# Performance work log

Measured on AMD Instinct MI355X. Metric: run time of the kernel, lower is better.

Reference implementation:

```python
import jax, jax.numpy as jnp
import numpy as np
from jax import lax

I_CH = 3
C_CH = 2 * I_CH            # 6
PAIRS = [(i, j) for i in range(C_CH) for j in range(i + 1, C_CH)]  # 15 Givens pairs


def _encoder(x, W, b_enc):
    # CMEncoder stand-in: single SAME 3x3 conv in_channels -> out_channels
    y = lax.conv_general_dilated(x, W, (1, 1), 'SAME',
                                 dimension_numbers=('NCHW', 'OIHW', 'NCHW'))
    return y + b_enc[None, :, None, None]


def _covariance_matrix(s, a):
    # s: [b,C,h,w] per-pixel variances; a: [b,15,h,w] Givens angles
    d = jnp.moveaxis(s, 1, -1)      # [b,h,w,C]
    ang = jnp.moveaxis(a, 1, -1)    # [b,h,w,15]
    b, h, w, Cc = d.shape
    R = jnp.broadcast_to(jnp.eye(Cc, dtype=d.dtype), (b, h, w, Cc, Cc))
    for k, (i, j) in enumerate(PAIRS):
        c = jnp.cos(ang[..., k])[..., None]
        sn = jnp.sin(ang[..., k])[..., None]
        ci = R[..., :, i]
        cj = R[..., :, j]
        R = R.at[..., :, i].set(c * ci + sn * cj)
        R = R.at[..., :, j].set(-sn * ci + c * cj)
    # S = R diag(d) R^T  -> [b,h,w,C,C]
    S = jnp.einsum('bhwmk,bhwk,bhwnk->bhwmn', R, d, R)
    return S, R, d


def reference(x, W, b_enc):
    I = I_CH
    C = C_CH
    p = _encoder(x, W, b_enc)              # [b,30,h,w]
    m = p[:, :C]                           # means [b,6,h,w]
    s = p[:, C:2 * C]
    s = jnp.square(jax.nn.relu(s) - jax.nn.relu(-s))
    s = jnp.clip(s, 1e-6)
    a = 2.0 * jnp.pi * jax.nn.sigmoid(p[:, 2 * C:-I])
    xf = p[:, -I:]                         # [b,3,h,w]
    S, R, d = _covariance_matrix(s, a)
    # S^{-1} = R diag(1/d) R^T (D diagonal, R orthogonal) -> [b,h,w,6,6]
    S_1 = jnp.einsum('bhwmk,bhwk,bhwnk->bhwmn', R, 1.0 / d, R)
    Sxx = S_1[..., :I, :I]
    Syx = S_1[..., I:, :I]
    Q = jnp.matmul(Syx, jnp.linalg.inv(Sxx))   # [b,h,w,3,3]
    mx = m[:, :I]
    my = m[:, I:]
    y = my + jnp.einsum('bijmn,bnij->bmij', Q, xf - mx)
    Sout = jnp.transpose(S, (0, 3, 4, 1, 2))   # [b,6,6,h,w]
    return (xf, m, Sout, y)


def setup_inputs() -> dict:
    key = jax.random.key(0)
    k1, k2, k3 = jax.random.split(key, 3)
    x = jax.random.normal(k1, (4, 3, 256, 256), dtype=jnp.float32)
    W = jax.random.normal(k2, (30, 3, 3, 3), dtype=jnp.float32) * 0.1
    b_enc = jax.random.normal(k3, (30,), dtype=jnp.float32) * 0.1
    return {'x': x, 'W': W, 'b_enc': b_enc}
```

## Files before the change

### kernel.cpp

```cpp
#include <hip/hip_runtime.h>
#include <math.h>

#define HWp 65536

typedef float v2f __attribute__((ext_vector_type(2)));

__device__ __forceinline__ v2f fma2(v2f a, v2f b, v2f c) {
    return __builtin_elementwise_fma(a, b, c);
}

__global__ __launch_bounds__(128, 6)
void gp_encoder_kernel(const float* __restrict__ x,
                       const float* __restrict__ Wt,
                       const float* __restrict__ be,
                       float* __restrict__ out)
{
    __shared__ float Dsh[6][64];
    __shared__ float Ssh[18][64];

    const int lane = threadIdx.x & 63;
    const int wid  = threadIdx.x >> 6;

    const int blk  = blockIdx.x;
    const int b    = blk >> 10;
    const int pixb = (blk & 1023) << 6;
    const int h    = pixb >> 8;
    const int w0   = pixb & 255;

    const bool wlo_ok = !(w0 == 0   && lane == 0);
    const bool whi_ok = !(w0 == 192 && lane == 63);
    const int  idx_m1 = wlo_ok ? lane - 1 : lane;
    const int  idx_p1 = whi_ok ? lane + 1 : lane;

    float xs[27];
    const float* xb = x + b * 3 * HWp;
    #pragma unroll
    for (int ci = 0; ci < 3; ++ci) {
        #pragma unroll
        for (int kh = 0; kh < 3; ++kh) {
            const int hh = h + kh - 1;
            float v0 = 0.f, v1 = 0.f, v2 = 0.f;
            if ((unsigned)hh < 256u) {
                const float* rp = xb + ci * HWp + hh * 256 + w0;
                v0 = rp[idx_m1];
                v1 = rp[lane];
                v2 = rp[idx_p1];
                v0 = wlo_ok ? v0 : 0.f;
                v2 = whi_ok ? v2 : 0.f;
            }
            xs[ci*9 + kh*3 + 0] = v0;
            xs[ci*9 + kh*3 + 1] = v1;
            xs[ci*9 + kh*3 + 2] = v2;
        }
    }
    v2f xp[13];
    #pragma unroll
    for (int q = 0; q < 13; ++q)
        xp[q] = (v2f){xs[2*q], xs[2*q + 1]};
    const float x26 = xs[26];

    float* out_xf = out                      + b*3*HWp  + pixb;
    float* out_m  = out + 4*3*HWp            + b*6*HWp  + pixb;
    float* out_S  = out + (4*3+4*6)*HWp      + b*36*HWp + pixb;
    float* out_y  = out + (4*3+4*6+4*36)*HWp + b*3*HWp  + pixb;

    float pb[15];

    if (wid == 0) {
        float pa[15];
        #pragma unroll
        for (int o = 0; o < 15; ++o) {
            const int base = (12 + o) * 27;
            v2f acc2 = (v2f){0.f, 0.f};
            #pragma unroll
            for (int q = 0; q < 13; ++q) {
                v2f wq;
                wq.x = Wt[base + 2*q];
                wq.y = Wt[base + 2*q + 1];
                acc2 = fma2(xp[q], wq, acc2);
            }
            const float r = be[12 + o] + acc2.x + acc2.y;
            pa[o] = fmaf(x26, Wt[base + 26], r);
        }

        v2f Rc[6][3];
        #pragma unroll
        for (int c = 0; c < 6; ++c)
            #pragma unroll
            for (int p = 0; p < 3; ++p)
                Rc[c][p] = (v2f){(2*p == c) ? 1.f : 0.f, (2*p + 1 == c) ? 1.f : 0.f};

        const int PI_[15] = {0,0,0,0,0,1,1,1,1,2,2,2,3,3,4};
        const int PJ_[15] = {1,2,3,4,5,2,3,4,5,3,4,5,4,5,5};
        #pragma unroll
        for (int k = 0; k < 15; ++k) {
            const int i = PI_[k], j = PJ_[k];
            const float e  = __expf(-pa[k]);
            const float sg = __builtin_amdgcn_rcpf(1.f + e);
            const float c  = __builtin_amdgcn_cosf(sg);
            const float sn = __builtin_amdgcn_sinf(sg);
            const v2f c2 = (v2f){c, c};
            const v2f s2 = (v2f){sn, sn};
            #pragma unroll
            for (int p = 0; p < 3; ++p) {
                const v2f ri = Rc[i][p], rj = Rc[j][p];
                Rc[i][p] = fma2(c2, ri, s2 * rj);
                Rc[j][p] = fma2(c2, rj, -(s2 * ri));
            }
        }

        __syncthreads();

        float dk[6];
        #pragma unroll
        for (int k = 0; k < 6; ++k)
            dk[k] = Dsh[k][lane];

        #pragma unroll
        for (int n = 0; n < 6; ++n) {
            float t[6];
            #pragma unroll
            for (int k = 0; k < 6; ++k) {
                const float rnk = (n & 1) ? Rc[k][n >> 1].y : Rc[k][n >> 1].x;
                t[k] = dk[k] * rnk;
            }
            v2f col[3];
            #pragma unroll
            for (int p = 0; p < 3; ++p) {
                v2f acc = Rc[0][p] * (v2f){t[0], t[0]};
                #pragma unroll
                for (int k = 1; k < 6; ++k)
                    acc = fma2(Rc[k][p], (v2f){t[k], t[k]}, acc);
                col[p] = acc;
            }
            #pragma unroll
            for (int p = 0; p < 3; ++p) {
                out_S[((2*p    )*6 + n)*HWp + lane] = col[p].x;
                out_S[((2*p + 1)*6 + n)*HWp + lane] = col[p].y;
            }
            Ssh[n*3 + 0][lane] = col[1].y;
            Ssh[n*3 + 1][lane] = col[2].x;
            Ssh[n*3 + 2][lane] = col[2].y;
        }

        __syncthreads();
    } else {
        #pragma unroll
        for (int o = 0; o < 15; ++o) {
            const int ch   = (o < 12) ? o : (o + 15);
            const int base = ch * 27;
            v2f acc2 = (v2f){0.f, 0.f};
            #pragma unroll
            for (int q = 0; q < 13; ++q) {
                v2f wq;
                wq.x = Wt[base + 2*q];
                wq.y = Wt[base + 2*q + 1];
                acc2 = fma2(xp[q], wq, acc2);
            }
            const float r = be[ch] + acc2.x + acc2.y;
            pb[o] = fmaf(x26, Wt[base + 26], r);
        }

        #pragma unroll
        for (int c = 0; c < 6; ++c)
            out_m[c*HWp + lane] = pb[c];
        #pragma unroll
        for (int i = 0; i < 3; ++i)
            out_xf[i*HWp + lane] = pb[12 + i];

        #pragma unroll
        for (int k = 0; k < 6; ++k) {
            const float s = pb[6 + k];
            Dsh[k][lane] = fmaxf(s * s, 1e-6f);
        }

        __syncthreads();
        __syncthreads();

        float syxf[3][3], syyf[3][3];
        #pragma unroll
        for (int c = 0; c < 3; ++c)
            #pragma unroll
            for (int r = 0; r < 3; ++r) {
                syxf[r][c] = Ssh[c*3 + r][lane];
                syyf[r][c] = Ssh[(3 + c)*3 + r][lane];
            }

        const double a00 = (double)syyf[0][0], a01 = (double)syyf[0][1], a02 = (double)syyf[0][2];
        const double a10 = (double)syyf[1][0], a11 = (double)syyf[1][1], a12 = (double)syyf[1][2];
        const double a20 = (double)syyf[2][0], a21 = (double)syyf[2][1], a22 = (double)syyf[2][2];

        const double det = a00*(a11*a22 - a12*a21)
                         - a01*(a10*a22 - a12*a20)
                         + a02*(a10*a21 - a11*a20);
        const double idet = 1.0 / det;

        double inv[3][3];
        inv[0][0] =  (a11*a22 - a12*a21) * idet;
        inv[0][1] = -(a01*a22 - a02*a21) * idet;
        inv[0][2] =  (a01*a12 - a02*a11) * idet;
        inv[1][0] = -(a10*a22 - a12*a20) * idet;
        inv[1][1] =  (a00*a22 - a02*a20) * idet;
        inv[1][2] = -(a00*a12 - a02*a10) * idet;
        inv[2][0] =  (a10*a21 - a11*a20) * idet;
        inv[2][1] = -(a00*a21 - a01*a20) * idet;
        inv[2][2] =  (a00*a11 - a01*a10) * idet;

        double Qp[3][3];
        #pragma unroll
        for (int r = 0; r < 3; ++r)
            #pragma unroll
            for (int c = 0; c < 3; ++c) {
                double acc = 0.0;
                #pragma unroll
                for (int k = 0; k < 3; ++k)
                    acc = fma(inv[r][k], (double)syxf[k][c], acc);
                Qp[r][c] = acc;
            }

        #pragma unroll
        for (int i = 0; i < 3; ++i) {
            double acc = (double)pb[3 + i];
            #pragma unroll
            for (int n = 0; n < 3; ++n)
                acc = fma(-Qp[i][n], (double)pb[12 + n] - (double)pb[n], acc);
            out_y[i*HWp + lane] = (float)acc;
        }
    }
}

extern "C" void kernel_launch(void* const* d_in, const int* in_sizes, int n_in,
                              void* d_out, int out_size, void* d_ws, size_t ws_size,
                              hipStream_t stream) {
    const float* x  = (const float*)d_in[0];
    const float* Wt = (const float*)d_in[1];
    const float* be = (const float*)d_in[2];
    float* out = (float*)d_out;

    dim3 grid(4096);
    dim3 block(128);
    hipLaunchKernelGGL(gp_encoder_kernel, grid, block, 0, stream, x, Wt, be, out);
}
```

Before: 23.99 us.

## Process two pixels per lane with packed math, symmetric S, and nontemporal stores

Each lane now handles two adjacent pixels, so the block covers 128 pixels and the grid is halved. The conv uses packed FMAs across the pixel pair, and R is stored row-major as a full 6x6. Only the upper triangle of S is computed and then mirrored, and all outputs go out as 8-byte nontemporal stores. The aim is to cut per-pixel instruction, load and store counts, at the cost of higher register pressure (launch_bounds occupancy hint dropped) and a serialized per-pixel double-precision solve.

Result: faster. 21.72 us (-9.5%).

```diff
diff --git a/kernel.cpp b/kernel.cpp
--- a/kernel.cpp
+++ b/kernel.cpp
@@ -8,224 +8,223 @@
 __device__ __forceinline__ v2f fma2(v2f a, v2f b, v2f c) {
     return __builtin_elementwise_fma(a, b, c);
 }
-
-__global__ __launch_bounds__(128, 6)
+__device__ __forceinline__ void stream_st2(float* p, v2f v) {
+    __builtin_nontemporal_store(v, (v2f*)p);
+}
+__device__ __forceinline__ float vget(v2f v, int px) { return px ? v.y : v.x; }
+
+__global__ __launch_bounds__(128)
 void gp_encoder_kernel(const float* __restrict__ x,
                        const float* __restrict__ Wt,
                        const float* __restrict__ be,
                        float* __restrict__ out)
 {
-    __shared__ float Dsh[6][64];
-    __shared__ float Ssh[18][64];
+    __shared__ v2f Dsh[6][64];
+    __shared__ v2f Ssh[18][64];
 
     const int lane = threadIdx.x & 63;
     const int wid  = threadIdx.x >> 6;
 
     const int blk  = blockIdx.x;
-    const int b    = blk >> 10;
-    const int pixb = (blk & 1023) << 6;
+    const int b    = blk >> 9;
+    const int pixb = (blk & 511) << 7;
     const int h    = pixb >> 8;
     const int w0   = pixb & 255;
 
+    const int  c0     = 2 * lane;
     const bool wlo_ok = !(w0 == 0   && lane == 0);
-    const bool whi_ok = !(w0 == 192 && lane == 63);
-    const int  idx_m1 = wlo_ok ? lane - 1 : lane;
-    const int  idx_p1 = whi_ok ? lane + 1 : lane;
-
-    float xs[27];
+    const bool whi_ok = !(w0 == 128 && lane == 63);
+    const int  idx_l  = wlo_ok ? c0 - 1 : c0;
+    const int  idx_r  = whi_ok ? c0 + 2 : c0;
+
+    v2f tp[27];
     const float* xb = x + b * 3 * HWp;
     #pragma unroll
     for (int ci = 0; ci < 3; ++ci) {
         #pragma unroll
         for (int kh = 0; kh < 3; ++kh) {
             const int hh = h + kh - 1;
-            float v0 = 0.f, v1 = 0.f, v2 = 0.f;
+            float lv = 0.f, rv = 0.f;
+            v2f   mv = (v2f){0.f, 0.f};
             if ((unsigned)hh < 256u) {
                 const float* rp = xb + ci * HWp + hh * 256 + w0;
-                v0 = rp[idx_m1];
-                v1 = rp[lane];
-                v2 = rp[idx_p1];
-                v0 = wlo_ok ? v0 : 0.f;
-                v2 = whi_ok ? v2 : 0.f;
-            }
-            xs[ci*9 + kh*3 + 0] = v0;
-            xs[ci*9 + kh*3 + 1] = v1;
-            xs[ci*9 + kh*3 + 2] = v2;
+                mv = *reinterpret_cast<const v2f*>(rp + c0);
+                lv = rp[idx_l];
+                rv = rp[idx_r];
+                lv = wlo_ok ? lv : 0.f;
+                rv = whi_ok ? rv : 0.f;
+            }
+            tp[ci*9 + kh*3 + 0] = (v2f){lv, mv.x};
+            tp[ci*9 + kh*3 + 1] = mv;
+            tp[ci*9 + kh*3 + 2] = (v2f){mv.y, rv};
         }
     }
-    v2f xp[13];
-    #pragma unroll
-    for (int q = 0; q < 13; ++q)
-        xp[q] = (v2f){xs[2*q], xs[2*q + 1]};
-    const float x26 = xs[26];
+
+    auto conv_ch = [&](int ch) -> v2f {
+        const float bb = be[ch];
+        v2f acc = (v2f){bb, bb};
+        const float* wp = Wt + ch * 27;
+        #pragma unroll
+        for (int t = 0; t < 27; ++t) {
+            const float wt = wp[t];
+            acc = fma2(tp[t], (v2f){wt, wt}, acc);
+        }
+        return acc;
+    };
 
     float* out_xf = out                      + b*3*HWp  + pixb;
     float* out_m  = out + 4*3*HWp            + b*6*HWp  + pixb;
     float* out_S  = out + (4*3+4*6)*HWp      + b*36*HWp + pixb;
     float* out_y  = out + (4*3+4*6+4*36)*HWp + b*3*HWp  + pixb;
 
-    float pb[15];
-
     if (wid == 0) {
-        float pa[15];
-        #pragma unroll
-        for (int o = 0; o < 15; ++o) {
-            const int base = (12 + o) * 27;
-            v2f acc2 = (v2f){0.f, 0.f};
-            #pragma unroll
-            for (int q = 0; q < 13; ++q) {
-                v2f wq;
-                wq.x = Wt[base + 2*q];
-                wq.y = Wt[base + 2*q + 1];
-                acc2 = fma2(xp[q], wq, acc2);
-            }
-            const float r = be[12 + o] + acc2.x + acc2.y;
-            pa[o] = fmaf(x26, Wt[base + 26], r);
-        }
-
-        v2f Rc[6][3];
-        #pragma unroll
-        for (int c = 0; c < 6; ++c)
-            #pragma unroll
-            for (int p = 0; p < 3; ++p)
-                Rc[c][p] = (v2f){(2*p == c) ? 1.f : 0.f, (2*p + 1 == c) ? 1.f : 0.f};
+        v2f pa[15];
+        #pragma unroll
+        for (int o = 0; o < 15; ++o)
+            pa[o] = conv_ch(12 + o);
+
+        v2f cs[15], ss[15];
+        #pragma unroll
+        for (int k = 0; k < 15; ++k) {
+            const float e0 = __expf(-pa[k].x);
+            const float e1 = __expf(-pa[k].y);
+            const float g0 = __builtin_amdgcn_rcpf(1.f + e0);
+            const float g1 = __builtin_amdgcn_rcpf(1.f + e1);
+            cs[k] = (v2f){__builtin_amdgcn_cosf(g0), __builtin_amdgcn_cosf(g1)};
+            ss[k] = (v2f){__builtin_amdgcn_sinf(g0), __builtin_amdgcn_sinf(g1)};
+        }
+
+        v2f R[6][6];
+        #pragma unroll
+        for (int r = 0; r < 6; ++r)
+            #pragma unroll
+            for (int c = 0; c < 6; ++c)
+                R[r][c] = (r == c) ? (v2f){1.f, 1.f} : (v2f){0.f, 0.f};
 
         const int PI_[15] = {0,0,0,0,0,1,1,1,1,2,2,2,3,3,4};
         const int PJ_[15] = {1,2,3,4,5,2,3,4,5,3,4,5,4,5,5};
         #pragma unroll
         for (int k = 0; k < 15; ++k) {
             const int i = PI_[k], j = PJ_[k];
-            const float e  = __expf(-pa[k]);
-            const float sg = __builtin_amdgcn_rcpf(1.f + e);
-            const float c  = __builtin_amdgcn_cosf(sg);
-            const float sn = __builtin_amdgcn_sinf(sg);
-            const v2f c2 = (v2f){c, c};
-            const v2f s2 = (v2f){sn, sn};
-            #pragma unroll
-            for (int p = 0; p < 3; ++p) {
-                const v2f ri = Rc[i][p], rj = Rc[j][p];
-                Rc[i][p] = fma2(c2, ri, s2 * rj);
-                Rc[j][p] = fma2(c2, rj, -(s2 * ri));
-            }
-        }
-
-        __syncthreads();
-
-        float dk[6];
+            const v2f c2 = cs[k], s2 = ss[k];
+            #pragma unroll
+            for (int r = 0; r < 6; ++r) {
+                const v2f ri = R[r][i], rj = R[r][j];
+                R[r][i] = fma2(c2, ri, s2 * rj);
+                R[r][j] = fma2(c2, rj, -(s2 * ri));
+            }
+        }
+
+        __syncthreads();
+
+        v2f dk[6];
         #pragma unroll
         for (int k = 0; k < 6; ++k)
             dk[k] = Dsh[k][lane];
 
         #pragma unroll
         for (int n = 0; n < 6; ++n) {
-            float t[6];
-            #pragma unroll
-            for (int k = 0; k < 6; ++k) {
-                const float rnk = (n & 1) ? Rc[k][n >> 1].y : Rc[k][n >> 1].x;
-                t[k] = dk[k] * rnk;
-            }
-            v2f col[3];
-            #pragma unroll
-            for (int p = 0; p < 3; ++p) {
-                v2f acc = Rc[0][p] * (v2f){t[0], t[0]};
+            v2f t[6];
+            #pragma unroll
+            for (int k = 0; k < 6; ++k)
+                t[k] = dk[k] * R[n][k];
+            #pragma unroll
+            for (int r = n; r < 6; ++r) {
+                v2f acc = t[0] * R[r][0];
                 #pragma unroll
                 for (int k = 1; k < 6; ++k)
-                    acc = fma2(Rc[k][p], (v2f){t[k], t[k]}, acc);
-                col[p] = acc;
-            }
-            #pragma unroll
-            for (int p = 0; p < 3; ++p) {
-                out_S[((2*p    )*6 + n)*HWp + lane] = col[p].x;
-                out_S[((2*p + 1)*6 + n)*HWp + lane] = col[p].y;
-            }
-            Ssh[n*3 + 0][lane] = col[1].y;
-            Ssh[n*3 + 1][lane] = col[2].x;
-            Ssh[n*3 + 2][lane] = col[2].y;
+                    acc = fma2(t[k], R[r][k], acc);
+                stream_st2(&out_S[(r*6 + n)*HWp + c0], acc);
+                if (r != n)
+                    stream_st2(&out_S[(n*6 + r)*HWp + c0], acc);
+                if (r >= 3)           Ssh[n*3 + (r-3)][lane] = acc;
+                if (n >= 3 && r != n) Ssh[r*3 + (n-3)][lane] = acc;
+            }
         }
 
         __syncthreads();
     } else {
-        #pragma unroll
-        for (int o = 0; o < 15; ++o) {
-            const int ch   = (o < 12) ? o : (o + 15);
-            const int base = ch * 27;
-            v2f acc2 = (v2f){0.f, 0.f};
-            #pragma unroll
-            for (int q = 0; q < 13; ++q) {
-                v2f wq;
-                wq.x = Wt[base + 2*q];
-                wq.y = Wt[base + 2*q + 1];
-                acc2 = fma2(xp[q], wq, acc2);
-            }
-            const float r = be[ch] + acc2.x + acc2.y;
-            pb[o] = fmaf(x26, Wt[base + 26], r);
-        }
+        v2f pbm[6], pbs[6], pxf[3];
+        #pragma unroll
+        for (int o = 0; o < 6; ++o) pbm[o] = conv_ch(o);
+        #pragma unroll
+        for (int o = 0; o < 6; ++o) pbs[o] = conv_ch(6 + o);
+        #pragma unroll
+        for (int o = 0; o < 3; ++o) pxf[o] = conv_ch(27 + o);
 
         #pragma unroll
         for (int c = 0; c < 6; ++c)
-            out_m[c*HWp + lane] = pb[c];
+            stream_st2(&out_m[c*HWp + c0], pbm[c]);
         #pragma unroll
         for (int i = 0; i < 3; ++i)
-            out_xf[i*HWp + lane] = pb[12 + i];
+            stream_st2(&out_xf[i*HWp + c0], pxf[i]);
 
         #pragma unroll
         for (int k = 0; k < 6; ++k) {
-            const float s = pb[6 + k];
-            Dsh[k][lane] = fmaxf(s * s, 1e-6f);
-        }
-
-        __syncthreads();
-        __syncthreads();
-
-        float syxf[3][3], syyf[3][3];
+            const v2f s = pbs[k];
+            Dsh[k][lane] = __builtin_elementwise_max(s * s, (v2f){1e-6f, 1e-6f});
+        }
+
+        __syncthreads();
+        __syncthreads();
+
+        v2f syx2[3][3], syy2[3][3];
         #pragma unroll
         for (int c = 0; c < 3; ++c)
             #pragma unroll
             for (int r = 0; r < 3; ++r) {
-                syxf[r][c] = Ssh[c*3 + r][lane];
-                syyf[r][c] = Ssh[(3 + c)*3 + r][lane];
-            }
-
-        const double a00 = (double)syyf[0][0], a01 = (double)syyf[0][1], a02 = (double)syyf[0][2];
-        const double a10 = (double)syyf[1][0], a11 = (double)syyf[1][1], a12 = (double)syyf[1][2];
-        const double a20 = (double)syyf[2][0], a21 = (double)syyf[2][1], a22 = (double)syyf[2][2];
-
-        const double det = a00*(a11*a22 - a12*a21)
-                         - a01*(a10*a22 - a12*a20)
-                         + a02*(a10*a21 - a11*a20);
-        const double idet = 1.0 / det;
-
-        double inv[3][3];
-        inv[0][0] =  (a11*a22 - a12*a21) * idet;
-        inv[0][1] = -(a01*a22 - a02*a21) * idet;
-        inv[0][2] =  (a01*a12 - a02*a11) * idet;
-        inv[1][0] = -(a10*a22 - a12*a20) * idet;
-        inv[1][1] =  (a00*a22 - a02*a20) * idet;
-        inv[1][2] = -(a00*a12 - a02*a10) * idet;
-        inv[2][0] =  (a10*a21 - a11*a20) * idet;
-        inv[2][1] = -(a00*a21 - a01*a20) * idet;
-        inv[2][2] =  (a00*a11 - a01*a10) * idet;
-
-        double Qp[3][3];
-        #pragma unroll
-        for (int r = 0; r < 3; ++r)
-            #pragma unroll
-            for (int c = 0; c < 3; ++c) {
-                double acc = 0.0;
+                syx2[r][c] = Ssh[c*3 + r][lane];
+                syy2[r][c] = Ssh[(3 + c)*3 + r][lane];
+            }
+
+        float yv[2][3];
+        #pragma unroll
+        for (int px = 0; px < 2; ++px) {
+            const double a00 = (double)vget(syy2[0][0], px), a01 = (double)vget(syy2[0][1], px), a02 = (double)vget(syy2[0][2], px);
+            const double a10 = (double)vget(syy2[1][0], px), a11 = (double)vget(syy2[1][1], px), a12 = (double)vget(syy2[1][2], px);
+            const double a20 = (double)vget(syy2[2][0], px), a21 = (double)vget(syy2[2][1], px), a22 = (double)vget(syy2[2][2], px);
+
+            const double det = a00*(a11*a22 - a12*a21)
+                             - a01*(a10*a22 - a12*a20)
+                             + a02*(a10*a21 - a11*a20);
+            const double idet = 1.0 / det;
+
+            double inv[3][3];
+            inv[0][0] =  (a11*a22 - a12*a21) * idet;
+            inv[0][1] = -(a01*a22 - a02*a21) * idet;
+            inv[0][2] =  (a01*a12 - a02*a11) * idet;
+            inv[1][0] = -(a10*a22 - a12*a20) * idet;
+            inv[1][1] =  (a00*a22 - a02*a20) * idet;
+            inv[1][2] = -(a00*a12 - a02*a10) * idet;
+            inv[2][0] =  (a10*a21 - a11*a20) * idet;
+            inv[2][1] = -(a00*a21 - a01*a20) * idet;
+            inv[2][2] =  (a00*a11 - a01*a10) * idet;
+
+            double Qp[3][3];
+            #pragma unroll
+            for (int r = 0; r < 3; ++r)
                 #pragma unroll
-                for (int k = 0; k < 3; ++k)
-                    acc = fma(inv[r][k], (double)syxf[k][c], acc);
-                Qp[r][c] = acc;
-            }
-
-        #pragma unroll
-        for (int i = 0; i < 3; ++i) {
-            double acc = (double)pb[3 + i];
-            #pragma unroll
-            for (int n = 0; n < 3; ++n)
-                acc = fma(-Qp[i][n], (double)pb[12 + n] - (double)pb[n], acc);
-            out_y[i*HWp + lane] = (float)acc;
-        }
+                for (int c = 0; c < 3; ++c) {
+                    double acc = 0.0;
+                    #pragma unroll
+                    for (int k = 0; k < 3; ++k)
+                        acc = fma(inv[r][k], (double)vget(syx2[k][c], px), acc);
+                    Qp[r][c] = acc;
+                }
+
+            #pragma unroll
+            for (int i = 0; i < 3; ++i) {
+                double acc = (double)vget(pbm[3 + i], px);
+                #pragma unroll
+                for (int n = 0; n < 3; ++n)
+                    acc = fma(-Qp[i][n], (double)vget(pxf[n], px) - (double)vget(pbm[n], px), acc);
+                yv[px][i] = (float)acc;
+            }
+        }
+
+        #pragma unroll
+        for (int i = 0; i < 3; ++i)
+            stream_st2(&out_y[i*HWp + c0], (v2f){yv[0][i], yv[1][i]});
     }
 }
 
@@ -237,7 +236,7 @@
     const float* be = (const float*)d_in[2];
     float* out = (float*)d_out;
 
-    dim3 grid(4096);
+    dim3 grid(2048);
     dim3 block(128);
     hipLaunchKernelGGL(gp_encoder_kernel, grid, block, 0, stream, x, Wt, be, out);
 }
```
